# Optimization experiments

Hardware: AMD Instinct MI355X
Metric: run time of the kernel (lower is better)

Reference implementation:

```python
import jax, jax.numpy as jnp
from jax import lax
import numpy as np

LATENT = 16
HIDDEN = 16  # latent_dim > 8 -> 16
NUM_ATTRACTORS = 64
GRAVITY = 0.01
INPUT_DIM = 300
B, S = 32, 2048
N_ITERS = 20


def setup_inputs() -> dict:
    key = jax.random.key(0)
    ks = jax.random.split(key, 12)
    sc = lambda fan_in: 1.0 / np.sqrt(fan_in)
    return {
        "inputs": jax.random.normal(ks[0], (B, S, INPUT_DIM), dtype=jnp.float32),
        "enc_w1": jax.random.normal(ks[1], (INPUT_DIM, HIDDEN), dtype=jnp.float32) * sc(INPUT_DIM),
        "enc_b1": jnp.zeros((HIDDEN,), dtype=jnp.float32),
        "enc_w2": jax.random.normal(ks[2], (HIDDEN, LATENT), dtype=jnp.float32) * sc(HIDDEN),
        "enc_b2": jnp.zeros((LATENT,), dtype=jnp.float32),
        "attractors": jax.random.normal(ks[3], (NUM_ATTRACTORS, LATENT), dtype=jnp.float32) * 0.1,
        "dec_w1": jax.random.normal(ks[4], (LATENT, HIDDEN), dtype=jnp.float32) * sc(LATENT),
        "dec_b1": jnp.zeros((HIDDEN,), dtype=jnp.float32),
        "dec_w2": jax.random.normal(ks[5], (HIDDEN, INPUT_DIM), dtype=jnp.float32) * sc(HIDDEN),
        "dec_b2": jnp.zeros((INPUT_DIM,), dtype=jnp.float32),
        "mass_w": jax.random.normal(ks[6], (LATENT, 1), dtype=jnp.float32) * sc(LATENT),
        "mass_b": jnp.zeros((1,), dtype=jnp.float32),
    }


def reference(inputs, enc_w1, enc_b1, enc_w2, enc_b2, attractors,
              dec_w1, dec_b1, dec_w2, dec_b2, mass_w, mass_b):
    b, s, _ = inputs.shape
    # encoder: Linear(300,16) -> ReLU -> Linear(16,latent)
    h = jax.nn.relu(jnp.einsum('bsi,ih->bsh', inputs, enc_w1) + enc_b1)
    emb = jnp.einsum('bsh,hd->bsd', h, enc_w2) + enc_b2  # [B,S,D]

    def step(pos, _):
        # pos: [B,S,D]; attractors: [A,D]
        diff = attractors[None, None, :, :] - pos[:, :, None, :]          # [B,S,A,D]
        dist = jnp.sqrt(jnp.sum(diff * diff, axis=-1, keepdims=True)) + 1e-6
        forces = jnp.sum(GRAVITY * diff / (dist * dist), axis=2)          # [B,S,D]
        new_pos = pos + 0.1 * forces
        change = jnp.sqrt(jnp.sum((new_pos - pos) ** 2))
        return new_pos, change

    # torch code breaks if change < 1e-6; with random data this never fires,
    # so the fixed 20-iteration scan is equivalent.
    positions, changes = lax.scan(step, emb, None, length=N_ITERS)

    attractor_field = positions.mean(axis=1)                              # [B,D]
    rec = jax.nn.relu(attractor_field @ dec_w1 + dec_b1) @ dec_w2 + dec_b2  # [B,300]
    reconstructions = jnp.broadcast_to(rec[:, None, :], (b, s, INPUT_DIM))
    masses = jax.nn.sigmoid(attractor_field @ mass_w + mass_b)            # [B,1]
    final_change = changes[-1]
    return attractor_field, reconstructions, masses, final_change
```

## Files before the change

### kernel.cpp

```cpp
#include <hip/hip_runtime.h>
#include <cmath>

#define BB 32
#define SS 2048
#define IND 300
#define HID 16
#define LAT 16
#define NA 64
#define NITER 20
#define GRAV 0.01f

#define OFF_FIELD 0
#define OFF_REC   512
#define OFF_MASS  (512 + BB*SS*IND)
#define OFF_CHG   (OFF_MASS + BB)

#define WS_FIELD 0
#define WS_CHG   512
#define WS_REC   1024

typedef __attribute__((ext_vector_type(8))) __bf16 bf16x8;
typedef __attribute__((ext_vector_type(4))) __bf16 bf16x4;
typedef __attribute__((ext_vector_type(4))) float f32x4;

#define WTS 80

__global__ __launch_bounds__(256, 1)
void k_enc_grav(const float* __restrict__ x, const float* __restrict__ w1,
                const float* __restrict__ b1, const float* __restrict__ w2,
                const float* __restrict__ b2, const float* __restrict__ att,
                float* __restrict__ ws)
{
    __shared__ __align__(16) char smem[4 * 64 * (HID + 1) * 4];
    float  (*hred)[64][HID + 1] = (float(*)[64][HID + 1])smem;
    __bf16* Wl = (__bf16*)smem;

    const int tid  = threadIdx.x;
    const int wave = tid >> 6, lane = tid & 63;
    const int quad = lane >> 4, col = lane & 15;
    const int tok0 = blockIdx.x * 64;

    {
        const int tl = tid & 63;
        const int ck = tid >> 6;
        const int base = ck * 76;
        const float* xrow = x + (size_t)(tok0 + tl) * IND + base;
        float h[HID];
        #pragma unroll
        for (int j = 0; j < HID; ++j) h[j] = 0.f;
        #pragma unroll 6
        for (int i = 0; i < 18; ++i) {
            f32x4 xv = *(const f32x4*)(xrow + i * 4);
            const float* wr = w1 + (base + i * 4) * HID;
            #pragma unroll
            for (int c = 0; c < 4; ++c)
                #pragma unroll
                for (int j = 0; j < HID; ++j)
                    h[j] = fmaf(xv[c], wr[c * HID + j], h[j]);
        }
        if (ck < 3) {
            f32x4 xv = *(const f32x4*)(xrow + 72);
            const float* wr = w1 + (base + 72) * HID;
            #pragma unroll
            for (int c = 0; c < 4; ++c)
                #pragma unroll
                for (int j = 0; j < HID; ++j)
                    h[j] = fmaf(xv[c], wr[c * HID + j], h[j]);
        }
        #pragma unroll
        for (int j = 0; j < HID; ++j) hred[ck][tl][j] = h[j];
    }
    __syncthreads();
    {
        const int tl = tid & 63;
        const int jg = (tid >> 6) * 4;
        #pragma unroll
        for (int jj = 0; jj < 4; ++jj) {
            const int j = jg + jj;
            float s = (hred[0][tl][j] + hred[1][tl][j]) +
                      (hred[2][tl][j] + hred[3][tl][j]);
            hred[0][tl][j] = fmaxf(s + b1[j], 0.f);
        }
    }
    __syncthreads();

    f32x4 p;
    {
        const float* hrow = &hred[0][wave * 16 + col][0];
        f32x4 acc = *(const f32x4*)(b2 + quad * 4);
        #pragma unroll
        for (int j = 0; j < HID; ++j) {
            float hj = hrow[j];
            f32x4 wv = *(const f32x4*)(w2 + j * LAT + quad * 4);
            #pragma unroll
            for (int r = 0; r < 4; ++r) acc[r] = fmaf(hj, wv[r], acc[r]);
        }
        p = acc;
    }
    __syncthreads();

    const f32x4 zf = {0.f, 0.f, 0.f, 0.f};
    bf16x8 ones8;
    #pragma unroll
    for (int e = 0; e < 8; ++e) ones8[e] = (__bf16)1.0f;

    bf16x8 aS[4];
    #pragma unroll
    for (int i = 0; i < 4; ++i) {
        f32x4 av = *(const f32x4*)(att + (16 * i + col) * LAT + quad * 4);
        #pragma unroll
        for (int m = 0; m < 4; ++m) {
            aS[i][2 * m]     = (__bf16)(-2.0f * av[m]);
            aS[i][2 * m + 1] = (__bf16)1.0f;
        }
    }
    f32x4 sanv[4];
    {
        float nrm[4];
        #pragma unroll
        for (int i = 0; i < 4; ++i) {
            const float* ar = att + (16 * i + col) * LAT;
            float s = 0.f;
            #pragma unroll
            for (int k = 0; k < LAT; ++k) s = fmaf(ar[k], ar[k], s);
            nrm[i] = s;
        }
        #pragma unroll
        for (int i = 0; i < 4; ++i)
            #pragma unroll
            for (int r = 0; r < 4; ++r)
                sanv[i][r] = __shfl(nrm[i], 16 * quad + quad * 4 + r);
    }
    bf16x8 aF[2];
    #pragma unroll
    for (int h = 0; h < 2; ++h)
        #pragma unroll
        for (int j = 0; j < 8; ++j)
            aF[h][j] = (__bf16)att[(32 * h + quad * 8 + j) * LAT + col];

    __bf16* myW = Wl + wave * 16 * WTS;

    float cd = 0.f;
    #pragma unroll 1
    for (int it = 0; it < NITER; ++it) {
        bf16x8 bp;
        #pragma unroll
        for (int m = 0; m < 4; ++m) {
            float v = p[m];
            bp[2 * m]     = (__bf16)v;
            bp[2 * m + 1] = (__bf16)(v * v);
        }
        f32x4 sf[4];
        #pragma unroll
        for (int i = 0; i < 4; ++i)
            sf[i] = __builtin_amdgcn_mfma_f32_16x16x32_bf16(aS[i], bp, zf, 0, 0, 0);

        #pragma unroll
        for (int i = 0; i < 4; ++i) {
            f32x4 s = sf[i];
            bf16x4 wp;
            #pragma unroll
            for (int r = 0; r < 4; ++r)
                wp[r] = (__bf16)__builtin_amdgcn_rcpf(s[r] + sanv[i][r]);
            *(bf16x4*)(myW + col * WTS + 16 * i + quad * 4) = wp;
        }
        bf16x8 bw0 = *(bf16x8*)(myW + col * WTS + quad * 8);
        bf16x8 bw1 = *(bf16x8*)(myW + col * WTS + 32 + quad * 8);

        f32x4 F  = __builtin_amdgcn_mfma_f32_16x16x32_bf16(aF[0], bw0, zf, 0, 0, 0);
        F  = __builtin_amdgcn_mfma_f32_16x16x32_bf16(aF[1], bw1, F,  0, 0, 0);
        f32x4 F2 = __builtin_amdgcn_mfma_f32_16x16x32_bf16(ones8, bw0, zf, 0, 0, 0);
        F2 = __builtin_amdgcn_mfma_f32_16x16x32_bf16(ones8, bw1, F2, 0, 0, 0);

        const bool last = (it == NITER - 1);
        #pragma unroll
        for (int r = 0; r < 4; ++r) {
            float np = fmaf(p[r], fmaf(F2[r], -0.1f * GRAV, 1.0f),
                            (0.1f * GRAV) * F[r]);
            if (last) { float d = np - p[r]; cd = fmaf(d, d, cd); }
            p[r] = np;
        }
    }

    f32x4 fs = p;
    #pragma unroll
    for (int m = 1; m <= 8; m <<= 1)
        #pragma unroll
        for (int r = 0; r < 4; ++r) fs[r] += __shfl_xor(fs[r], m);
    const int b = blockIdx.x >> 5;
    if (col == 0) {
        #pragma unroll
        for (int r = 0; r < 4; ++r)
            atomicAdd(ws + WS_FIELD + b * LAT + quad * 4 + r, fs[r]);
    }

    float c2 = cd;
    c2 += __shfl_xor(c2, 1);  c2 += __shfl_xor(c2, 2);  c2 += __shfl_xor(c2, 4);
    c2 += __shfl_xor(c2, 8);  c2 += __shfl_xor(c2, 16); c2 += __shfl_xor(c2, 32);
    if (lane == 0) atomicAdd(ws + WS_CHG, c2);
}

__global__ __launch_bounds__(512)
void k_finalize(const float* __restrict__ dw1, const float* __restrict__ db1,
                const float* __restrict__ dw2, const float* __restrict__ db2,
                const float* __restrict__ mw,  const float* __restrict__ mb,
                float* __restrict__ ws, float* __restrict__ out)
{
    __shared__ float sf[LAT];
    __shared__ float sh[HID];
    const int b = blockIdx.x, t = threadIdx.x;
    if (t < LAT) {
        float f = ws[WS_FIELD + b * LAT + t] * (1.f / SS);
        sf[t] = f;
        out[OFF_FIELD + b * LAT + t] = f;
    }
    __syncthreads();
    if (t < HID) {
        float a = db1[t];
        #pragma unroll
        for (int d = 0; d < LAT; ++d) a = fmaf(sf[d], dw1[d * HID + t], a);
        sh[t] = fmaxf(a, 0.f);
    }
    if (t == 32) {
        float a = mb[0];
        #pragma unroll
        for (int d = 0; d < LAT; ++d) a = fmaf(sf[d], mw[d], a);
        out[OFF_MASS + b] = 1.f / (1.f + expf(-a));
    }
    if (b == 0 && t == 33) out[OFF_CHG] = sqrtf(ws[WS_CHG]);
    __syncthreads();
    if (t < IND) {
        float a = db2[t];
        #pragma unroll
        for (int j = 0; j < HID; ++j) a = fmaf(sh[j], dw2[j * IND + t], a);
        ws[WS_REC + b * IND + t] = a;
    }
}

#define CHUNK 8192
#define CPB   (SS * IND / CHUNK)
__global__ __launch_bounds__(256)
void k_broadcast(const float* __restrict__ ws, float* __restrict__ out)
{
    const int b = blockIdx.x / CPB;
    const int c = blockIdx.x % CPB;
    const float* row = ws + WS_REC + b * IND;
    f32x4* o = (f32x4*)(out + OFF_REC + (size_t)b * (SS * IND) + (size_t)c * CHUNK);
    #pragma unroll
    for (int i = 0; i < CHUNK / 4 / 256; ++i) {
        const int o4 = i * 256 + threadIdx.x;
        const int r  = (c * CHUNK + o4 * 4) % IND;
        f32x4 v = *(const f32x4*)(row + r);
        __builtin_nontemporal_store(v, o + o4);
    }
}

extern "C" void kernel_launch(void* const* d_in, const int* in_sizes, int n_in,
                              void* d_out, int out_size, void* d_ws, size_t ws_size,
                              hipStream_t stream)
{
    const float* x   = (const float*)d_in[0];
    const float* ew1 = (const float*)d_in[1];
    const float* eb1 = (const float*)d_in[2];
    const float* ew2 = (const float*)d_in[3];
    const float* eb2 = (const float*)d_in[4];
    const float* att = (const float*)d_in[5];
    const float* dw1 = (const float*)d_in[6];
    const float* db1 = (const float*)d_in[7];
    const float* dw2 = (const float*)d_in[8];
    const float* db2 = (const float*)d_in[9];
    const float* mw  = (const float*)d_in[10];
    const float* mb  = (const float*)d_in[11];
    float* out = (float*)d_out;
    float* ws  = (float*)d_ws;

    (void)hipMemsetAsync(ws, 0, (WS_CHG + 1) * sizeof(float), stream);
    k_enc_grav<<<BB * SS / 64, 256, 0, stream>>>(x, ew1, eb1, ew2, eb2, att, ws);
    k_finalize<<<BB, 512, 0, stream>>>(dw1, db1, dw2, db2, mw, mb, ws, out);
    k_broadcast<<<BB * CPB, 256, 0, stream>>>(ws, out);
}
```

Before: 237.6 us.

## Split encoder and gravity kernels, double gravity ILP, fuse finalize into broadcast

The fused encoder+gravity kernel becomes two kernels. The encoder writes latent positions to a scratch area inside the output's reconstruction region. The gravity kernel then processes two 16-token sets per wave, so the two independent MFMA chains can interleave and hide latency, with half as many blocks. The decoder finalize step is folded into the broadcast kernel: each block recomputes the 300-wide row into shared memory, which removes one launch and the workspace round trip. This adds a global write and read of the positions and redundant per-block decoder math.

```diff
diff --git a/kernel.cpp b/kernel.cpp
--- a/kernel.cpp
+++ b/kernel.cpp
@@ -17,24 +17,19 @@
 
 #define WS_FIELD 0
 #define WS_CHG   512
-#define WS_REC   1024
 
 typedef __attribute__((ext_vector_type(8))) __bf16 bf16x8;
 typedef __attribute__((ext_vector_type(4))) __bf16 bf16x4;
 typedef __attribute__((ext_vector_type(4))) float f32x4;
 
-#define WTS 80
+#define WTS 88
 
 __global__ __launch_bounds__(256, 1)
-void k_enc_grav(const float* __restrict__ x, const float* __restrict__ w1,
-                const float* __restrict__ b1, const float* __restrict__ w2,
-                const float* __restrict__ b2, const float* __restrict__ att,
-                float* __restrict__ ws)
+void k_enc(const float* __restrict__ x, const float* __restrict__ w1,
+           const float* __restrict__ b1, const float* __restrict__ w2,
+           const float* __restrict__ b2, float* __restrict__ pbuf)
 {
-    __shared__ __align__(16) char smem[4 * 64 * (HID + 1) * 4];
-    float  (*hred)[64][HID + 1] = (float(*)[64][HID + 1])smem;
-    __bf16* Wl = (__bf16*)smem;
-
+    __shared__ float hred[4][64][HID + 1];
     const int tid  = threadIdx.x;
     const int wave = tid >> 6, lane = tid & 63;
     const int quad = lane >> 4, col = lane & 15;
@@ -83,8 +78,6 @@
         }
     }
     __syncthreads();
-
-    f32x4 p;
     {
         const float* hrow = &hred[0][wave * 16 + col][0];
         f32x4 acc = *(const f32x4*)(b2 + quad * 4);
@@ -95,9 +88,18 @@
             #pragma unroll
             for (int r = 0; r < 4; ++r) acc[r] = fmaf(hj, wv[r], acc[r]);
         }
-        p = acc;
-    }
-    __syncthreads();
+        ((f32x4*)pbuf)[(size_t)(tok0 + wave * 16 + col) * 4 + quad] = acc;
+    }
+}
+
+__global__ __launch_bounds__(256, 1)
+void k_grav(const float* __restrict__ att, const float* __restrict__ pbuf,
+            float* __restrict__ ws)
+{
+    __shared__ __bf16 Wl[4][2][16 * WTS];
+    const int tid  = threadIdx.x;
+    const int wave = tid >> 6, lane = tid & 63;
+    const int quad = lane >> 4, col = lane & 15;
 
     const f32x4 zf = {0.f, 0.f, 0.f, 0.f};
     bf16x8 ones8;
@@ -138,81 +140,104 @@
         for (int j = 0; j < 8; ++j)
             aF[h][j] = (__bf16)att[(32 * h + quad * 8 + j) * LAT + col];
 
-    __bf16* myW = Wl + wave * 16 * WTS;
+    const int t0 = blockIdx.x * 128 + wave * 32 + col;
+    f32x4 p[2];
+    p[0] = ((const f32x4*)pbuf)[(size_t)t0 * 4 + quad];
+    p[1] = ((const f32x4*)pbuf)[(size_t)(t0 + 16) * 4 + quad];
+
+    __bf16* myW[2] = { &Wl[wave][0][0], &Wl[wave][1][0] };
 
     float cd = 0.f;
     #pragma unroll 1
     for (int it = 0; it < NITER; ++it) {
-        bf16x8 bp;
-        #pragma unroll
-        for (int m = 0; m < 4; ++m) {
-            float v = p[m];
-            bp[2 * m]     = (__bf16)v;
-            bp[2 * m + 1] = (__bf16)(v * v);
-        }
-        f32x4 sf[4];
-        #pragma unroll
-        for (int i = 0; i < 4; ++i)
-            sf[i] = __builtin_amdgcn_mfma_f32_16x16x32_bf16(aS[i], bp, zf, 0, 0, 0);
-
-        #pragma unroll
-        for (int i = 0; i < 4; ++i) {
-            f32x4 s = sf[i];
-            bf16x4 wp;
-            #pragma unroll
-            for (int r = 0; r < 4; ++r)
-                wp[r] = (__bf16)__builtin_amdgcn_rcpf(s[r] + sanv[i][r]);
-            *(bf16x4*)(myW + col * WTS + 16 * i + quad * 4) = wp;
-        }
-        bf16x8 bw0 = *(bf16x8*)(myW + col * WTS + quad * 8);
-        bf16x8 bw1 = *(bf16x8*)(myW + col * WTS + 32 + quad * 8);
-
-        f32x4 F  = __builtin_amdgcn_mfma_f32_16x16x32_bf16(aF[0], bw0, zf, 0, 0, 0);
-        F  = __builtin_amdgcn_mfma_f32_16x16x32_bf16(aF[1], bw1, F,  0, 0, 0);
-        f32x4 F2 = __builtin_amdgcn_mfma_f32_16x16x32_bf16(ones8, bw0, zf, 0, 0, 0);
-        F2 = __builtin_amdgcn_mfma_f32_16x16x32_bf16(ones8, bw1, F2, 0, 0, 0);
+        bf16x8 bp[2];
+        #pragma unroll
+        for (int s = 0; s < 2; ++s)
+            #pragma unroll
+            for (int m = 0; m < 4; ++m) {
+                float v = p[s][m];
+                bp[s][2 * m]     = (__bf16)v;
+                bp[s][2 * m + 1] = (__bf16)(v * v);
+            }
+        f32x4 sf[2][4];
+        #pragma unroll
+        for (int s = 0; s < 2; ++s)
+            #pragma unroll
+            for (int i = 0; i < 4; ++i)
+                sf[s][i] = __builtin_amdgcn_mfma_f32_16x16x32_bf16(aS[i], bp[s], zf, 0, 0, 0);
+
+        #pragma unroll
+        for (int s = 0; s < 2; ++s)
+            #pragma unroll
+            for (int i = 0; i < 4; ++i) {
+                bf16x4 wp;
+                #pragma unroll
+                for (int r = 0; r < 4; ++r)
+                    wp[r] = (__bf16)__builtin_amdgcn_rcpf(sf[s][i][r] + sanv[i][r]);
+                *(bf16x4*)(myW[s] + col * WTS + 16 * i + quad * 4) = wp;
+            }
+        bf16x8 bw[2][2];
+        #pragma unroll
+        for (int s = 0; s < 2; ++s)
+            #pragma unroll
+            for (int h = 0; h < 2; ++h)
+                bw[s][h] = *(bf16x8*)(myW[s] + col * WTS + 32 * h + quad * 8);
 
         const bool last = (it == NITER - 1);
         #pragma unroll
-        for (int r = 0; r < 4; ++r) {
-            float np = fmaf(p[r], fmaf(F2[r], -0.1f * GRAV, 1.0f),
-                            (0.1f * GRAV) * F[r]);
-            if (last) { float d = np - p[r]; cd = fmaf(d, d, cd); }
-            p[r] = np;
-        }
-    }
-
-    f32x4 fs = p;
+        for (int s = 0; s < 2; ++s) {
+            f32x4 F  = __builtin_amdgcn_mfma_f32_16x16x32_bf16(aF[0], bw[s][0], zf, 0, 0, 0);
+            F  = __builtin_amdgcn_mfma_f32_16x16x32_bf16(aF[1], bw[s][1], F,  0, 0, 0);
+            f32x4 F2 = __builtin_amdgcn_mfma_f32_16x16x32_bf16(ones8, bw[s][0], zf, 0, 0, 0);
+            F2 = __builtin_amdgcn_mfma_f32_16x16x32_bf16(ones8, bw[s][1], F2, 0, 0, 0);
+            #pragma unroll
+            for (int r = 0; r < 4; ++r) {
+                float np = fmaf(p[s][r], fmaf(F2[r], -0.1f * GRAV, 1.0f),
+                                (0.1f * GRAV) * F[r]);
+                if (last) { float d = np - p[s][r]; cd = fmaf(d, d, cd); }
+                p[s][r] = np;
+            }
+        }
+    }
+
+    f32x4 fs;
+    #pragma unroll
+    for (int r = 0; r < 4; ++r) fs[r] = p[0][r] + p[1][r];
     #pragma unroll
     for (int m = 1; m <= 8; m <<= 1)
         #pragma unroll
         for (int r = 0; r < 4; ++r) fs[r] += __shfl_xor(fs[r], m);
-    const int b = blockIdx.x >> 5;
+    const int b = blockIdx.x >> 4;
     if (col == 0) {
         #pragma unroll
         for (int r = 0; r < 4; ++r)
             atomicAdd(ws + WS_FIELD + b * LAT + quad * 4 + r, fs[r]);
     }
-
     float c2 = cd;
     c2 += __shfl_xor(c2, 1);  c2 += __shfl_xor(c2, 2);  c2 += __shfl_xor(c2, 4);
     c2 += __shfl_xor(c2, 8);  c2 += __shfl_xor(c2, 16); c2 += __shfl_xor(c2, 32);
     if (lane == 0) atomicAdd(ws + WS_CHG, c2);
 }
 
-__global__ __launch_bounds__(512)
-void k_finalize(const float* __restrict__ dw1, const float* __restrict__ db1,
-                const float* __restrict__ dw2, const float* __restrict__ db2,
-                const float* __restrict__ mw,  const float* __restrict__ mb,
-                float* __restrict__ ws, float* __restrict__ out)
+#define CHUNK 8192
+#define CPB   (SS * IND / CHUNK)
+__global__ __launch_bounds__(256)
+void k_bcast(const float* __restrict__ dw1, const float* __restrict__ db1,
+             const float* __restrict__ dw2, const float* __restrict__ db2,
+             const float* __restrict__ mw,  const float* __restrict__ mb,
+             const float* __restrict__ ws, float* __restrict__ out)
 {
     __shared__ float sf[LAT];
     __shared__ float sh[HID];
-    const int b = blockIdx.x, t = threadIdx.x;
+    __shared__ __align__(16) float srow[IND];
+    const int blk = blockIdx.x;
+    const int b = blk / CPB, c = blk % CPB;
+    const int t = threadIdx.x;
+
     if (t < LAT) {
         float f = ws[WS_FIELD + b * LAT + t] * (1.f / SS);
         sf[t] = f;
-        out[OFF_FIELD + b * LAT + t] = f;
+        if (c == 0) out[OFF_FIELD + b * LAT + t] = f;
     }
     __syncthreads();
     if (t < HID) {
@@ -221,36 +246,37 @@
         for (int d = 0; d < LAT; ++d) a = fmaf(sf[d], dw1[d * HID + t], a);
         sh[t] = fmaxf(a, 0.f);
     }
-    if (t == 32) {
+    if (c == 0 && t == 32) {
         float a = mb[0];
         #pragma unroll
         for (int d = 0; d < LAT; ++d) a = fmaf(sf[d], mw[d], a);
         out[OFF_MASS + b] = 1.f / (1.f + expf(-a));
     }
-    if (b == 0 && t == 33) out[OFF_CHG] = sqrtf(ws[WS_CHG]);
-    __syncthreads();
-    if (t < IND) {
-        float a = db2[t];
-        #pragma unroll
-        for (int j = 0; j < HID; ++j) a = fmaf(sh[j], dw2[j * IND + t], a);
-        ws[WS_REC + b * IND + t] = a;
-    }
-}
-
-#define CHUNK 8192
-#define CPB   (SS * IND / CHUNK)
-__global__ __launch_bounds__(256)
-void k_broadcast(const float* __restrict__ ws, float* __restrict__ out)
-{
-    const int b = blockIdx.x / CPB;
-    const int c = blockIdx.x % CPB;
-    const float* row = ws + WS_REC + b * IND;
+    if (blk == 0 && t == 33) out[OFF_CHG] = sqrtf(ws[WS_CHG]);
+    __syncthreads();
+    {
+        float a = db2[t % IND];
+        if (t < IND) {
+            a = db2[t];
+            #pragma unroll
+            for (int j = 0; j < HID; ++j) a = fmaf(sh[j], dw2[j * IND + t], a);
+            srow[t] = a;
+        }
+        if (t < IND - 256) {
+            const int tc = t + 256;
+            float a2 = db2[tc];
+            #pragma unroll
+            for (int j = 0; j < HID; ++j) a2 = fmaf(sh[j], dw2[j * IND + tc], a2);
+            srow[tc] = a2;
+        }
+    }
+    __syncthreads();
     f32x4* o = (f32x4*)(out + OFF_REC + (size_t)b * (SS * IND) + (size_t)c * CHUNK);
     #pragma unroll
     for (int i = 0; i < CHUNK / 4 / 256; ++i) {
-        const int o4 = i * 256 + threadIdx.x;
+        const int o4 = i * 256 + t;
         const int r  = (c * CHUNK + o4 * 4) % IND;
-        f32x4 v = *(const f32x4*)(row + r);
+        f32x4 v = *(const f32x4*)(srow + r);
         __builtin_nontemporal_store(v, o + o4);
     }
 }
@@ -273,9 +299,10 @@
     const float* mb  = (const float*)d_in[11];
     float* out = (float*)d_out;
     float* ws  = (float*)d_ws;
+    float* pbuf = out + OFF_REC;
 
     (void)hipMemsetAsync(ws, 0, (WS_CHG + 1) * sizeof(float), stream);
-    k_enc_grav<<<BB * SS / 64, 256, 0, stream>>>(x, ew1, eb1, ew2, eb2, att, ws);
-    k_finalize<<<BB, 512, 0, stream>>>(dw1, db1, dw2, db2, mw, mb, ws, out);
-    k_broadcast<<<BB * CPB, 256, 0, stream>>>(ws, out);
+    k_enc <<<BB * SS / 64, 256, 0, stream>>>(x, ew1, eb1, ew2, eb2, pbuf);
+    k_grav<<<BB * SS / 128, 256, 0, stream>>>(att, pbuf, ws);
+    k_bcast<<<BB * CPB, 256, 0, stream>>>(dw1, db1, dw2, db2, mw, mb, ws, out);
 }
```

Result: slower. 256.1 us (+7.8%).

## Use bf16 MFMA for encoder matmuls and fuse finalize into broadcast

Applied to the files above, without the earlier changes.

The encoder's 300x16 and 16x16 linear layers now run as bf16 MFMA instructions. Each block first stages its 64 input rows as bf16 in shared memory, replacing the per-thread scalar FMA loops and the cross-wave reduction. The separate finalize kernel is folded into the broadcast kernel, so every broadcast block recomputes the small decoder row into shared memory and one launch disappears. In exchange, the encoder now rounds inputs and weights to bf16, which lowers precision, and the decoder work is repeated redundantly in every broadcast block.

```diff
diff --git a/kernel.cpp b/kernel.cpp
--- a/kernel.cpp
+++ b/kernel.cpp
@@ -17,13 +17,14 @@
 
 #define WS_FIELD 0
 #define WS_CHG   512
-#define WS_REC   1024
 
 typedef __attribute__((ext_vector_type(8))) __bf16 bf16x8;
 typedef __attribute__((ext_vector_type(4))) __bf16 bf16x4;
 typedef __attribute__((ext_vector_type(4))) float f32x4;
 
-#define WTS 80
+#define XST 328
+#define HST 40
+#define WTS 88
 
 __global__ __launch_bounds__(256, 1)
 void k_enc_grav(const float* __restrict__ x, const float* __restrict__ w1,
@@ -31,8 +32,9 @@
                 const float* __restrict__ b2, const float* __restrict__ att,
                 float* __restrict__ ws)
 {
-    __shared__ __align__(16) char smem[4 * 64 * (HID + 1) * 4];
-    float  (*hred)[64][HID + 1] = (float(*)[64][HID + 1])smem;
+    __shared__ __align__(16) char smem[64 * XST * 2 + 4 * 16 * HST * 2];
+    __bf16* xs = (__bf16*)smem;
+    __bf16* hl = (__bf16*)(smem + 64 * XST * 2);
     __bf16* Wl = (__bf16*)smem;
 
     const int tid  = threadIdx.x;
@@ -41,61 +43,65 @@
     const int tok0 = blockIdx.x * 64;
 
     {
-        const int tl = tid & 63;
-        const int ck = tid >> 6;
-        const int base = ck * 76;
-        const float* xrow = x + (size_t)(tok0 + tl) * IND + base;
-        float h[HID];
-        #pragma unroll
-        for (int j = 0; j < HID; ++j) h[j] = 0.f;
-        #pragma unroll 6
-        for (int i = 0; i < 18; ++i) {
-            f32x4 xv = *(const f32x4*)(xrow + i * 4);
-            const float* wr = w1 + (base + i * 4) * HID;
-            #pragma unroll
-            for (int c = 0; c < 4; ++c)
+        const f32x4* xg = (const f32x4*)(x + (size_t)tok0 * IND);
+        #pragma unroll
+        for (int i = 0; i < 19; ++i) {
+            const int idx = i * 256 + tid;
+            if (idx < 4800) {
+                f32x4 v = xg[idx];
+                const int row = idx / 75, c4 = idx - row * 75;
+                bf16x4 b;
                 #pragma unroll
-                for (int j = 0; j < HID; ++j)
-                    h[j] = fmaf(xv[c], wr[c * HID + j], h[j]);
-        }
-        if (ck < 3) {
-            f32x4 xv = *(const f32x4*)(xrow + 72);
-            const float* wr = w1 + (base + 72) * HID;
-            #pragma unroll
-            for (int c = 0; c < 4; ++c)
-                #pragma unroll
-                for (int j = 0; j < HID; ++j)
-                    h[j] = fmaf(xv[c], wr[c * HID + j], h[j]);
-        }
-        #pragma unroll
-        for (int j = 0; j < HID; ++j) hred[ck][tl][j] = h[j];
-    }
-    __syncthreads();
-    {
-        const int tl = tid & 63;
-        const int jg = (tid >> 6) * 4;
-        #pragma unroll
-        for (int jj = 0; jj < 4; ++jj) {
-            const int j = jg + jj;
-            float s = (hred[0][tl][j] + hred[1][tl][j]) +
-                      (hred[2][tl][j] + hred[3][tl][j]);
-            hred[0][tl][j] = fmaxf(s + b1[j], 0.f);
-        }
-    }
-    __syncthreads();
+                for (int e = 0; e < 4; ++e) b[e] = (__bf16)v[e];
+                *(bf16x4*)(xs + row * XST + c4 * 4) = b;
+            }
+        }
+        if (tid < 64) {
+            #pragma unroll
+            for (int c = 0; c < 20; ++c) xs[tid * XST + 300 + c] = (__bf16)0.f;
+        }
+    }
+
+    bf16x8 w1f[10];
+    #pragma unroll
+    for (int s = 0; s < 10; ++s)
+        #pragma unroll
+        for (int j = 0; j < 8; ++j) {
+            const int k = s * 32 + quad * 8 + j;
+            w1f[s][j] = (k < IND) ? (__bf16)w1[k * HID + col] : (__bf16)0.f;
+        }
+    __syncthreads();
+
+    {
+        const float b1c = b1[col];
+        f32x4 hacc = {b1c, b1c, b1c, b1c};
+        const __bf16* myx = xs + (wave * 16 + col) * XST + quad * 8;
+        #pragma unroll
+        for (int s = 0; s < 10; ++s) {
+            bf16x8 af = *(const bf16x8*)(myx + s * 32);
+            hacc = __builtin_amdgcn_mfma_f32_16x16x32_bf16(af, w1f[s], hacc, 0, 0, 0);
+        }
+        __bf16* myh = hl + wave * 16 * HST;
+        #pragma unroll
+        for (int r = 0; r < 4; ++r)
+            myh[(quad * 4 + r) * HST + col] = (__bf16)fmaxf(hacc[r], 0.f);
+    }
 
     f32x4 p;
     {
-        const float* hrow = &hred[0][wave * 16 + col][0];
-        f32x4 acc = *(const f32x4*)(b2 + quad * 4);
-        #pragma unroll
-        for (int j = 0; j < HID; ++j) {
-            float hj = hrow[j];
-            f32x4 wv = *(const f32x4*)(w2 + j * LAT + quad * 4);
-            #pragma unroll
-            for (int r = 0; r < 4; ++r) acc[r] = fmaf(hj, wv[r], acc[r]);
-        }
-        p = acc;
+        bf16x8 w2tf;
+        #pragma unroll
+        for (int j = 0; j < 8; ++j) {
+            const int k = quad * 8 + j;
+            w2tf[j] = (k < HID) ? (__bf16)w2[k * LAT + col] : (__bf16)0.f;
+        }
+        bf16x8 bh;
+        #pragma unroll
+        for (int e = 0; e < 8; ++e) bh[e] = (__bf16)0.f;
+        if (quad < 2)
+            bh = *(const bf16x8*)(hl + wave * 16 * HST + col * HST + quad * 8);
+        f32x4 pacc = *(const f32x4*)(b2 + quad * 4);
+        p = __builtin_amdgcn_mfma_f32_16x16x32_bf16(w2tf, bh, pacc, 0, 0, 0);
     }
     __syncthreads();
 
@@ -157,11 +163,10 @@
 
         #pragma unroll
         for (int i = 0; i < 4; ++i) {
-            f32x4 s = sf[i];
             bf16x4 wp;
             #pragma unroll
             for (int r = 0; r < 4; ++r)
-                wp[r] = (__bf16)__builtin_amdgcn_rcpf(s[r] + sanv[i][r]);
+                wp[r] = (__bf16)__builtin_amdgcn_rcpf(sf[i][r] + sanv[i][r]);
             *(bf16x4*)(myW + col * WTS + 16 * i + quad * 4) = wp;
         }
         bf16x8 bw0 = *(bf16x8*)(myW + col * WTS + quad * 8);
@@ -193,26 +198,31 @@
         for (int r = 0; r < 4; ++r)
             atomicAdd(ws + WS_FIELD + b * LAT + quad * 4 + r, fs[r]);
     }
-
     float c2 = cd;
     c2 += __shfl_xor(c2, 1);  c2 += __shfl_xor(c2, 2);  c2 += __shfl_xor(c2, 4);
     c2 += __shfl_xor(c2, 8);  c2 += __shfl_xor(c2, 16); c2 += __shfl_xor(c2, 32);
     if (lane == 0) atomicAdd(ws + WS_CHG, c2);
 }
 
-__global__ __launch_bounds__(512)
-void k_finalize(const float* __restrict__ dw1, const float* __restrict__ db1,
-                const float* __restrict__ dw2, const float* __restrict__ db2,
-                const float* __restrict__ mw,  const float* __restrict__ mb,
-                float* __restrict__ ws, float* __restrict__ out)
+#define CHUNK 8192
+#define CPB   (SS * IND / CHUNK)
+__global__ __launch_bounds__(256)
+void k_bcast(const float* __restrict__ dw1, const float* __restrict__ db1,
+             const float* __restrict__ dw2, const float* __restrict__ db2,
+             const float* __restrict__ mw,  const float* __restrict__ mb,
+             const float* __restrict__ ws, float* __restrict__ out)
 {
     __shared__ float sf[LAT];
     __shared__ float sh[HID];
-    const int b = blockIdx.x, t = threadIdx.x;
+    __shared__ __align__(16) float srow[IND];
+    const int blk = blockIdx.x;
+    const int b = blk / CPB, c = blk % CPB;
+    const int t = threadIdx.x;
+
     if (t < LAT) {
         float f = ws[WS_FIELD + b * LAT + t] * (1.f / SS);
         sf[t] = f;
-        out[OFF_FIELD + b * LAT + t] = f;
+        if (c == 0) out[OFF_FIELD + b * LAT + t] = f;
     }
     __syncthreads();
     if (t < HID) {
@@ -221,36 +231,34 @@
         for (int d = 0; d < LAT; ++d) a = fmaf(sf[d], dw1[d * HID + t], a);
         sh[t] = fmaxf(a, 0.f);
     }
-    if (t == 32) {
+    if (c == 0 && t == 32) {
         float a = mb[0];
         #pragma unroll
         for (int d = 0; d < LAT; ++d) a = fmaf(sf[d], mw[d], a);
         out[OFF_MASS + b] = 1.f / (1.f + expf(-a));
     }
-    if (b == 0 && t == 33) out[OFF_CHG] = sqrtf(ws[WS_CHG]);
+    if (blk == 0 && t == 33) out[OFF_CHG] = sqrtf(ws[WS_CHG]);
     __syncthreads();
     if (t < IND) {
         float a = db2[t];
         #pragma unroll
         for (int j = 0; j < HID; ++j) a = fmaf(sh[j], dw2[j * IND + t], a);
-        ws[WS_REC + b * IND + t] = a;
-    }
-}
-
-#define CHUNK 8192
-#define CPB   (SS * IND / CHUNK)
-__global__ __launch_bounds__(256)
-void k_broadcast(const float* __restrict__ ws, float* __restrict__ out)
-{
-    const int b = blockIdx.x / CPB;
-    const int c = blockIdx.x % CPB;
-    const float* row = ws + WS_REC + b * IND;
+        srow[t] = a;
+    }
+    if (t < IND - 256) {
+        const int tc = t + 256;
+        float a2 = db2[tc];
+        #pragma unroll
+        for (int j = 0; j < HID; ++j) a2 = fmaf(sh[j], dw2[j * IND + tc], a2);
+        srow[tc] = a2;
+    }
+    __syncthreads();
     f32x4* o = (f32x4*)(out + OFF_REC + (size_t)b * (SS * IND) + (size_t)c * CHUNK);
     #pragma unroll
     for (int i = 0; i < CHUNK / 4 / 256; ++i) {
-        const int o4 = i * 256 + threadIdx.x;
+        const int o4 = i * 256 + t;
         const int r  = (c * CHUNK + o4 * 4) % IND;
-        f32x4 v = *(const f32x4*)(row + r);
+        f32x4 v = *(const f32x4*)(srow + r);
         __builtin_nontemporal_store(v, o + o4);
     }
 }
@@ -276,6 +284,5 @@
 
     (void)hipMemsetAsync(ws, 0, (WS_CHG + 1) * sizeof(float), stream);
     k_enc_grav<<<BB * SS / 64, 256, 0, stream>>>(x, ew1, eb1, ew2, eb2, att, ws);
-    k_finalize<<<BB, 512, 0, stream>>>(dw1, db1, dw2, db2, mw, mb, ws, out);
-    k_broadcast<<<BB * CPB, 256, 0, stream>>>(ws, out);
+    k_bcast<<<BB * CPB, 256, 0, stream>>>(dw1, db1, dw2, db2, mw, mb, ws, out);
 }
```

New measurement: 234.0 us. About the same (-1.5%).
